# Performance work log

Hardware: AMD Instinct MI355X
Metric: run time of the kernel (lower is better)

Reference implementation:

```python
import jax, jax.numpy as jnp
import numpy as np

B, L, S, H, E, D = 4, 2048, 2048, 8, 64, 64

def setup_inputs() -> dict:
    key = jax.random.key(0)
    kq, kk, kv = jax.random.split(key, 3)
    queries = jax.random.normal(kq, (B, L, H, E), dtype=jnp.float32)
    keys = jax.random.normal(kk, (B, S, H, E), dtype=jnp.float32)
    values = jax.random.normal(kv, (B, S, H, D), dtype=jnp.float32)
    return {"queries": queries, "keys": keys, "values": values}

def reference(queries, keys, values):
    # scale = self.scale or 1/sqrt(E)
    scale = 1.0 / jnp.sqrt(jnp.float32(queries.shape[-1]))
    # scores: [B, H, L, S]
    scores = jnp.einsum('blhe,bshe->bhls', queries, keys)
    # dropout is identity at inference (Keras Dropout only active in training)
    A = jax.nn.softmax(scale * scores, axis=-1)
    # output: [B, L, H, D]
    return jnp.einsum('bhls,bshd->blhd', A, values)
```

## Files before the change

kernel.cpp:

```cpp
#include <hip/hip_runtime.h>


#define B_ 4
#define L_ 2048
#define S_ 2048
#define H_ 8
#define E_ 64
#define D_ 64

#define NUMSZ (B_ * L_ * H_ * D_)
#define LSZ (B_ * L_ * H_)
#define KVELEM (B_ * H_ * S_ * 64)
#define TILE_ELEMS 2048

typedef __attribute__((ext_vector_type(8))) __bf16 bf16x8;
typedef __attribute__((ext_vector_type(4))) __bf16 bf16x4;
typedef __attribute__((ext_vector_type(16))) float floatx16;

union BF4U { bf16x4 v; uint2 u; };
union BF8U { bf16x8 v; uint4 u; };

__device__ __forceinline__ void async_load16(const void* g, void* l) {
  __builtin_amdgcn_global_load_lds(
      (const __attribute__((address_space(1))) unsigned int*)g,
      (__attribute__((address_space(3))) unsigned int*)l, 16, 0, 0);
}

__device__ __forceinline__ bf16x8 cvt8(float4 a, float4 b) {
  bf16x8 r;
  r[0] = (__bf16)a.x; r[1] = (__bf16)a.y; r[2] = (__bf16)a.z; r[3] = (__bf16)a.w;
  r[4] = (__bf16)b.x; r[5] = (__bf16)b.y; r[6] = (__bf16)b.z; r[7] = (__bf16)b.w;
  return r;
}

__global__ __launch_bounds__(256) void prep_kernel(const float* __restrict__ K,
                                                   const float* __restrict__ V,
                                                   __bf16* __restrict__ Kb,
                                                   __bf16* __restrict__ Vb) {
  __shared__ float Vs[32 * 64];
  const int bid = blockIdx.x;
  const int tile = bid & 63;
  const int h = (bid >> 6) & 7;
  const int b = bid >> 9;
  const int s0 = tile * 32;
  const int i = threadIdx.x;

  {
    const int s = i >> 3, cp = i & 7;
    const int e0 = 8 * (cp ^ (s & 7));
    const float* src = K + (((size_t)(b * S_ + s0 + s) * H_ + h) * E_ + e0);
    float4 a = *(const float4*)src;
    float4 bb = *(const float4*)(src + 4);
    *(bf16x8*)(Kb + (size_t)bid * TILE_ELEMS + i * 8) = cvt8(a, bb);
  }
  {
    const int s = i >> 3, d0 = (i & 7) * 8;
    const float* src = V + (((size_t)(b * S_ + s0 + s) * H_ + h) * D_ + d0);
    float4 a = *(const float4*)src;
    float4 bb = *(const float4*)(src + 4);
    *(float4*)&Vs[s * 64 + d0] = a;
    *(float4*)&Vs[s * 64 + d0 + 4] = bb;
  }
  __syncthreads();
  {
    const int Ll = i >> 3, cp = i & 7;
    const int ci = cp ^ (Ll & 7);
    const int d = 2 * Ll + (ci >> 2);
    const int ch = ci & 3;
    BF8U o;
#pragma unroll
    for (int j = 0; j < 8; ++j) o.v[j] = (__bf16)Vs[(8 * ch + j) * 64 + d];
    *(bf16x8*)(Vb + (size_t)bid * TILE_ELEMS + i * 8) = o.v;
  }
}

__global__ __launch_bounds__(256, 4) void attn_kernel(const float* __restrict__ Q,
                                                      const __bf16* __restrict__ Kb,
                                                      const __bf16* __restrict__ Vb,
                                                      float* __restrict__ O,
                                                      float* __restrict__ num_ws,
                                                      float* __restrict__ l_ws,
                                                      int splits) {
  __shared__ __align__(16) __bf16 Kt[2][TILE_ELEMS];
  __shared__ __align__(16) __bf16 Vt[2][TILE_ELEMS];

  const int tid = threadIdx.x;
  const int lane = tid & 63;
  const int wave = tid >> 6;
  const int q32 = lane & 31;
  const int h32 = lane >> 5;

  const int bid = blockIdx.x;
  const int qb = bid & 15;
  const int h = (bid >> 4) & 7;
  const int b = (bid >> 7) & 3;
  const int split = bid >> 9;

  const int NT = (S_ / 32) / splits;
  const int tile0 = split * NT;

  const float qscale = 0.125f * 1.44269504088896340736f;
  const int qrow = qb * 128 + wave * 32 + q32;
  const float* qp = Q + ((size_t)(b * L_ + qrow) * H_ + h) * E_;
  bf16x8 qf[4];
#pragma unroll
  for (int c = 0; c < 4; ++c) {
    const float* p = qp + c * 16 + h32 * 8;
    float4 a = *(const float4*)p;
    float4 bb = *(const float4*)(p + 4);
    float t[8] = {a.x, a.y, a.z, a.w, bb.x, bb.y, bb.z, bb.w};
#pragma unroll
    for (int j = 0; j < 8; ++j) qf[c][j] = (__bf16)(t[j] * qscale);
  }

  int koff[4];
#pragma unroll
  for (int c = 0; c < 4; ++c) koff[c] = (q32 * 8 + (((2 * c + h32) ^ (q32 & 7)))) * 8;
  int voff[2][2];
#pragma unroll
  for (int s2 = 0; s2 < 2; ++s2)
#pragma unroll
    for (int dt = 0; dt < 2; ++dt) {
      int dp = dt * 32 + q32;
      int Ll = dp >> 1;
      int ci = (dp & 1) * 4 + 2 * s2 + h32;
      voff[s2][dt] = (Ll * 8 + (ci ^ (Ll & 7))) * 8;
    }

  float l = 0.0f;
  floatx16 ot[2];
#pragma unroll
  for (int r = 0; r < 16; ++r) { ot[0][r] = 0.f; ot[1][r] = 0.f; }

  const __bf16* KbBH = Kb + (size_t)((b * H_ + h) * 64) * TILE_ELEMS;
  const __bf16* VbBH = Vb + (size_t)((b * H_ + h) * 64) * TILE_ELEMS;
  const int lin8 = (wave * 64 + lane) * 8;

  async_load16(KbBH + (size_t)tile0 * TILE_ELEMS + lin8, &Kt[0][wave * 512]);
  async_load16(VbBH + (size_t)tile0 * TILE_ELEMS + lin8, &Vt[0][wave * 512]);

  for (int t = 0; t < NT; ++t) {
    const int buf = t & 1;
    __syncthreads();

    if (t + 1 < NT) {
      async_load16(KbBH + (size_t)(tile0 + t + 1) * TILE_ELEMS + lin8,
                   &Kt[buf ^ 1][wave * 512]);
      async_load16(VbBH + (size_t)(tile0 + t + 1) * TILE_ELEMS + lin8,
                   &Vt[buf ^ 1][wave * 512]);
    }

    floatx16 sc;
#pragma unroll
    for (int r = 0; r < 16; ++r) sc[r] = 0.f;
    {
      const __bf16* Kbuf = Kt[buf];
#pragma unroll
      for (int c = 0; c < 4; ++c) {
        bf16x8 kA = *(const bf16x8*)&Kbuf[koff[c]];
        sc = __builtin_amdgcn_mfma_f32_32x32x16_bf16(kA, qf[c], sc, 0, 0, 0);
      }
    }

    BF4U pg[4];
#pragma unroll
    for (int g = 0; g < 4; ++g) {
      float p0 = __builtin_amdgcn_exp2f(sc[4 * g + 0]);
      float p1 = __builtin_amdgcn_exp2f(sc[4 * g + 1]);
      float p2 = __builtin_amdgcn_exp2f(sc[4 * g + 2]);
      float p3 = __builtin_amdgcn_exp2f(sc[4 * g + 3]);
      l += (p0 + p1) + (p2 + p3);
      pg[g].v = (bf16x4){(__bf16)p0, (__bf16)p1, (__bf16)p2, (__bf16)p3};
    }
    uint2 sendA = h32 ? pg[0].u : pg[1].u;
    uint2 sendB = h32 ? pg[2].u : pg[3].u;
    uint2 recvA, recvB;
    recvA.x = __shfl_xor((int)sendA.x, 32);
    recvA.y = __shfl_xor((int)sendA.y, 32);
    recvB.x = __shfl_xor((int)sendB.x, 32);
    recvB.y = __shfl_xor((int)sendB.y, 32);
    BF8U pB0, pB1;
    if (h32 == 0) {
      pB0.u = (uint4){pg[0].u.x, pg[0].u.y, recvA.x, recvA.y};
      pB1.u = (uint4){pg[2].u.x, pg[2].u.y, recvB.x, recvB.y};
    } else {
      pB0.u = (uint4){recvA.x, recvA.y, pg[1].u.x, pg[1].u.y};
      pB1.u = (uint4){recvB.x, recvB.y, pg[3].u.x, pg[3].u.y};
    }

    {
      const __bf16* Vbuf = Vt[buf];
      bf16x8 vA00 = *(const bf16x8*)&Vbuf[voff[0][0]];
      bf16x8 vA01 = *(const bf16x8*)&Vbuf[voff[0][1]];
      bf16x8 vA10 = *(const bf16x8*)&Vbuf[voff[1][0]];
      bf16x8 vA11 = *(const bf16x8*)&Vbuf[voff[1][1]];
      ot[0] = __builtin_amdgcn_mfma_f32_32x32x16_bf16(vA00, pB0.v, ot[0], 0, 0, 0);
      ot[1] = __builtin_amdgcn_mfma_f32_32x32x16_bf16(vA01, pB0.v, ot[1], 0, 0, 0);
      ot[0] = __builtin_amdgcn_mfma_f32_32x32x16_bf16(vA10, pB1.v, ot[0], 0, 0, 0);
      ot[1] = __builtin_amdgcn_mfma_f32_32x32x16_bf16(vA11, pB1.v, ot[1], 0, 0, 0);
    }
  }

  l += __shfl_xor(l, 32);
  if (splits == 1) {
    const float inv = 1.0f / l;
    float* orow = O + ((size_t)(b * L_ + qrow) * H_ + h) * D_;
#pragma unroll
    for (int dt = 0; dt < 2; ++dt)
#pragma unroll
      for (int g = 0; g < 4; ++g) {
        float4 v = {ot[dt][4 * g + 0] * inv, ot[dt][4 * g + 1] * inv,
                    ot[dt][4 * g + 2] * inv, ot[dt][4 * g + 3] * inv};
        *(float4*)(orow + dt * 32 + g * 8 + h32 * 4) = v;
      }
  } else {
    float* nrow = num_ws + (size_t)split * NUMSZ + ((size_t)(b * L_ + qrow) * H_ + h) * D_;
#pragma unroll
    for (int dt = 0; dt < 2; ++dt)
#pragma unroll
      for (int g = 0; g < 4; ++g) {
        float4 v = {ot[dt][4 * g + 0], ot[dt][4 * g + 1], ot[dt][4 * g + 2],
                    ot[dt][4 * g + 3]};
        *(float4*)(nrow + dt * 32 + g * 8 + h32 * 4) = v;
      }
    if (h32 == 0) l_ws[(size_t)split * LSZ + (size_t)(b * L_ + qrow) * H_ + h] = l;
  }
}

__global__ __launch_bounds__(256) void combine_kernel(const float* __restrict__ num_ws,
                                                      const float* __restrict__ l_ws,
                                                      float* __restrict__ O, int splits) {
  const size_t i4 = ((size_t)blockIdx.x * 256 + threadIdx.x) * 4;
  float4 acc = {0.f, 0.f, 0.f, 0.f};
  float lt = 0.f;
  for (int s = 0; s < splits; ++s) {
    float4 v = *(const float4*)(num_ws + (size_t)s * NUMSZ + i4);
    acc.x += v.x; acc.y += v.y; acc.z += v.z; acc.w += v.w;
    lt += l_ws[(size_t)s * LSZ + (i4 >> 6)];
  }
  const float inv = 1.0f / lt;
  float4 o = {acc.x * inv, acc.y * inv, acc.z * inv, acc.w * inv};
  *(float4*)(O + i4) = o;
}

extern "C" void kernel_launch(void* const* d_in, const int* in_sizes, int n_in,
                              void* d_out, int out_size, void* d_ws, size_t ws_size,
                              hipStream_t stream) {
  const float* Q = (const float*)d_in[0];
  const float* K = (const float*)d_in[1];
  const float* V = (const float*)d_in[2];
  float* O = (float*)d_out;

  __bf16* Kb = (__bf16*)d_ws;
  __bf16* Vb = Kb + KVELEM;
  float* num_ws = (float*)(Vb + KVELEM);
  const size_t base = (size_t)2 * KVELEM * sizeof(__bf16);
  const size_t per_split = ((size_t)NUMSZ + (size_t)LSZ) * sizeof(float);
  int splits = 1;
  if (ws_size >= base + 4 * per_split) splits = 4;
  else if (ws_size >= base + 2 * per_split) splits = 2;
  float* l_ws = num_ws + (size_t)splits * NUMSZ;

  prep_kernel<<<B_ * H_ * 64, 256, 0, stream>>>(K, V, Kb, Vb);
  dim3 grid(B_ * H_ * (L_ / 128) * splits);
  attn_kernel<<<grid, 256, 0, stream>>>(Q, Kb, Vb, O, num_ws, l_ws, splits);
  if (splits > 1) {
    combine_kernel<<<NUMSZ / 4 / 256, 256, 0, stream>>>(num_ws, l_ws, O, splits);
  }
}
```

Measured before the change: 153.7 us.

## Process two K/V tiles per barrier with independent accumulators

Each loop iteration now loads and processes two 32-key K/V tiles instead of one. This halves the number of __syncthreads barriers and async-load issue points per split. Two separate output accumulator sets break the serial MFMA dependency chain between sub-tiles, and they are summed at the end. The cost is doubled LDS use and more accumulator registers, with launch bounds lowered from 4 to 3 blocks per CU, which may reduce occupancy. It also requires the per-split tile count to be even.

```diff
diff --git a/kernel.cpp b/kernel.cpp
--- a/kernel.cpp
+++ b/kernel.cpp
@@ -74,15 +74,15 @@
   }
 }
 
-__global__ __launch_bounds__(256, 4) void attn_kernel(const float* __restrict__ Q,
+__global__ __launch_bounds__(256, 3) void attn_kernel(const float* __restrict__ Q,
                                                       const __bf16* __restrict__ Kb,
                                                       const __bf16* __restrict__ Vb,
                                                       float* __restrict__ O,
                                                       float* __restrict__ num_ws,
                                                       float* __restrict__ l_ws,
                                                       int splits) {
-  __shared__ __align__(16) __bf16 Kt[2][TILE_ELEMS];
-  __shared__ __align__(16) __bf16 Vt[2][TILE_ELEMS];
+  __shared__ __align__(16) __bf16 Kt[2][2 * TILE_ELEMS];
+  __shared__ __align__(16) __bf16 Vt[2][2 * TILE_ELEMS];
 
   const int tid = threadIdx.x;
   const int lane = tid & 63;
@@ -96,8 +96,8 @@
   const int b = (bid >> 7) & 3;
   const int split = bid >> 9;
 
-  const int NT = (S_ / 32) / splits;
-  const int tile0 = split * NT;
+  const int NT2 = (S_ / 32) / splits / 2;
+  const int tile0 = split * NT2 * 2;
 
   const float qscale = 0.125f * 1.44269504088896340736f;
   const int qrow = qb * 128 + wave * 32 + q32;
@@ -128,80 +128,96 @@
     }
 
   float l = 0.0f;
-  floatx16 ot[2];
-#pragma unroll
-  for (int r = 0; r < 16; ++r) { ot[0][r] = 0.f; ot[1][r] = 0.f; }
+  floatx16 ot[2][2];
+#pragma unroll
+  for (int sb = 0; sb < 2; ++sb)
+#pragma unroll
+    for (int r = 0; r < 16; ++r) { ot[sb][0][r] = 0.f; ot[sb][1][r] = 0.f; }
 
   const __bf16* KbBH = Kb + (size_t)((b * H_ + h) * 64) * TILE_ELEMS;
   const __bf16* VbBH = Vb + (size_t)((b * H_ + h) * 64) * TILE_ELEMS;
   const int lin8 = (wave * 64 + lane) * 8;
 
-  async_load16(KbBH + (size_t)tile0 * TILE_ELEMS + lin8, &Kt[0][wave * 512]);
-  async_load16(VbBH + (size_t)tile0 * TILE_ELEMS + lin8, &Vt[0][wave * 512]);
-
-  for (int t = 0; t < NT; ++t) {
+#pragma unroll
+  for (int st = 0; st < 2; ++st) {
+    async_load16(KbBH + (size_t)(tile0 + st) * TILE_ELEMS + lin8,
+                 &Kt[0][st * TILE_ELEMS + wave * 512]);
+    async_load16(VbBH + (size_t)(tile0 + st) * TILE_ELEMS + lin8,
+                 &Vt[0][st * TILE_ELEMS + wave * 512]);
+  }
+
+  for (int t = 0; t < NT2; ++t) {
     const int buf = t & 1;
     __syncthreads();
 
-    if (t + 1 < NT) {
-      async_load16(KbBH + (size_t)(tile0 + t + 1) * TILE_ELEMS + lin8,
-                   &Kt[buf ^ 1][wave * 512]);
-      async_load16(VbBH + (size_t)(tile0 + t + 1) * TILE_ELEMS + lin8,
-                   &Vt[buf ^ 1][wave * 512]);
+    if (t + 1 < NT2) {
+#pragma unroll
+      for (int st = 0; st < 2; ++st) {
+        async_load16(KbBH + (size_t)(tile0 + 2 * (t + 1) + st) * TILE_ELEMS + lin8,
+                     &Kt[buf ^ 1][st * TILE_ELEMS + wave * 512]);
+        async_load16(VbBH + (size_t)(tile0 + 2 * (t + 1) + st) * TILE_ELEMS + lin8,
+                     &Vt[buf ^ 1][st * TILE_ELEMS + wave * 512]);
+      }
     }
 
-    floatx16 sc;
-#pragma unroll
-    for (int r = 0; r < 16; ++r) sc[r] = 0.f;
-    {
-      const __bf16* Kbuf = Kt[buf];
+#pragma unroll
+    for (int sb = 0; sb < 2; ++sb) {
+      const __bf16* Kbuf = &Kt[buf][sb * TILE_ELEMS];
+      const __bf16* Vbuf = &Vt[buf][sb * TILE_ELEMS];
+
+      floatx16 sc;
+#pragma unroll
+      for (int r = 0; r < 16; ++r) sc[r] = 0.f;
 #pragma unroll
       for (int c = 0; c < 4; ++c) {
         bf16x8 kA = *(const bf16x8*)&Kbuf[koff[c]];
         sc = __builtin_amdgcn_mfma_f32_32x32x16_bf16(kA, qf[c], sc, 0, 0, 0);
       }
-    }
-
-    BF4U pg[4];
-#pragma unroll
-    for (int g = 0; g < 4; ++g) {
-      float p0 = __builtin_amdgcn_exp2f(sc[4 * g + 0]);
-      float p1 = __builtin_amdgcn_exp2f(sc[4 * g + 1]);
-      float p2 = __builtin_amdgcn_exp2f(sc[4 * g + 2]);
-      float p3 = __builtin_amdgcn_exp2f(sc[4 * g + 3]);
-      l += (p0 + p1) + (p2 + p3);
-      pg[g].v = (bf16x4){(__bf16)p0, (__bf16)p1, (__bf16)p2, (__bf16)p3};
-    }
-    uint2 sendA = h32 ? pg[0].u : pg[1].u;
-    uint2 sendB = h32 ? pg[2].u : pg[3].u;
-    uint2 recvA, recvB;
-    recvA.x = __shfl_xor((int)sendA.x, 32);
-    recvA.y = __shfl_xor((int)sendA.y, 32);
-    recvB.x = __shfl_xor((int)sendB.x, 32);
-    recvB.y = __shfl_xor((int)sendB.y, 32);
-    BF8U pB0, pB1;
-    if (h32 == 0) {
-      pB0.u = (uint4){pg[0].u.x, pg[0].u.y, recvA.x, recvA.y};
-      pB1.u = (uint4){pg[2].u.x, pg[2].u.y, recvB.x, recvB.y};
-    } else {
-      pB0.u = (uint4){recvA.x, recvA.y, pg[1].u.x, pg[1].u.y};
-      pB1.u = (uint4){recvB.x, recvB.y, pg[3].u.x, pg[3].u.y};
-    }
-
-    {
-      const __bf16* Vbuf = Vt[buf];
+
+      BF4U pg[4];
+#pragma unroll
+      for (int g = 0; g < 4; ++g) {
+        float p0 = __builtin_amdgcn_exp2f(sc[4 * g + 0]);
+        float p1 = __builtin_amdgcn_exp2f(sc[4 * g + 1]);
+        float p2 = __builtin_amdgcn_exp2f(sc[4 * g + 2]);
+        float p3 = __builtin_amdgcn_exp2f(sc[4 * g + 3]);
+        l += (p0 + p1) + (p2 + p3);
+        pg[g].v = (bf16x4){(__bf16)p0, (__bf16)p1, (__bf16)p2, (__bf16)p3};
+      }
+      uint2 sendA = h32 ? pg[0].u : pg[1].u;
+      uint2 sendB = h32 ? pg[2].u : pg[3].u;
+      uint2 recvA, recvB;
+      recvA.x = __shfl_xor((int)sendA.x, 32);
+      recvA.y = __shfl_xor((int)sendA.y, 32);
+      recvB.x = __shfl_xor((int)sendB.x, 32);
+      recvB.y = __shfl_xor((int)sendB.y, 32);
+      BF8U pB0, pB1;
+      if (h32 == 0) {
+        pB0.u = (uint4){pg[0].u.x, pg[0].u.y, recvA.x, recvA.y};
+        pB1.u = (uint4){pg[2].u.x, pg[2].u.y, recvB.x, recvB.y};
+      } else {
+        pB0.u = (uint4){recvA.x, recvA.y, pg[1].u.x, pg[1].u.y};
+        pB1.u = (uint4){recvB.x, recvB.y, pg[3].u.x, pg[3].u.y};
+      }
+
       bf16x8 vA00 = *(const bf16x8*)&Vbuf[voff[0][0]];
       bf16x8 vA01 = *(const bf16x8*)&Vbuf[voff[0][1]];
       bf16x8 vA10 = *(const bf16x8*)&Vbuf[voff[1][0]];
       bf16x8 vA11 = *(const bf16x8*)&Vbuf[voff[1][1]];
-      ot[0] = __builtin_amdgcn_mfma_f32_32x32x16_bf16(vA00, pB0.v, ot[0], 0, 0, 0);
-      ot[1] = __builtin_amdgcn_mfma_f32_32x32x16_bf16(vA01, pB0.v, ot[1], 0, 0, 0);
-      ot[0] = __builtin_amdgcn_mfma_f32_32x32x16_bf16(vA10, pB1.v, ot[0], 0, 0, 0);
-      ot[1] = __builtin_amdgcn_mfma_f32_32x32x16_bf16(vA11, pB1.v, ot[1], 0, 0, 0);
+      ot[sb][0] = __builtin_amdgcn_mfma_f32_32x32x16_bf16(vA00, pB0.v, ot[sb][0], 0, 0, 0);
+      ot[sb][1] = __builtin_amdgcn_mfma_f32_32x32x16_bf16(vA01, pB0.v, ot[sb][1], 0, 0, 0);
+      ot[sb][0] = __builtin_amdgcn_mfma_f32_32x32x16_bf16(vA10, pB1.v, ot[sb][0], 0, 0, 0);
+      ot[sb][1] = __builtin_amdgcn_mfma_f32_32x32x16_bf16(vA11, pB1.v, ot[sb][1], 0, 0, 0);
     }
   }
 
   l += __shfl_xor(l, 32);
+  floatx16 om[2];
+#pragma unroll
+  for (int dt = 0; dt < 2; ++dt)
+#pragma unroll
+    for (int r = 0; r < 16; ++r) om[dt][r] = ot[0][dt][r] + ot[1][dt][r];
+
   if (splits == 1) {
     const float inv = 1.0f / l;
     float* orow = O + ((size_t)(b * L_ + qrow) * H_ + h) * D_;
@@ -209,8 +225,8 @@
     for (int dt = 0; dt < 2; ++dt)
 #pragma unroll
       for (int g = 0; g < 4; ++g) {
-        float4 v = {ot[dt][4 * g + 0] * inv, ot[dt][4 * g + 1] * inv,
-                    ot[dt][4 * g + 2] * inv, ot[dt][4 * g + 3] * inv};
+        float4 v = {om[dt][4 * g + 0] * inv, om[dt][4 * g + 1] * inv,
+                    om[dt][4 * g + 2] * inv, om[dt][4 * g + 3] * inv};
         *(float4*)(orow + dt * 32 + g * 8 + h32 * 4) = v;
       }
   } else {
@@ -219,8 +235,8 @@
     for (int dt = 0; dt < 2; ++dt)
 #pragma unroll
       for (int g = 0; g < 4; ++g) {
-        float4 v = {ot[dt][4 * g + 0], ot[dt][4 * g + 1], ot[dt][4 * g + 2],
-                    ot[dt][4 * g + 3]};
+        float4 v = {om[dt][4 * g + 0], om[dt][4 * g + 1], om[dt][4 * g + 2],
+                    om[dt][4 * g + 3]};
         *(float4*)(nrow + dt * 32 + g * 8 + h32 * 4) = v;
       }
     if (h32 == 0) l_ws[(size_t)split * LSZ + (size_t)(b * L_ + qrow) * H_ + h] = l;
```

New measurement: 154.8 us. No clear change (+0.7%).
